# Kernel tuning notes

Measured on AMD Instinct MI355X. Metric: run time of the kernel, lower is better.

The kernel has to match this reference:

```python
import math
import jax, jax.numpy as jnp
import numpy as np

HIDDEN = 1024
N_HEADS = 16
HEAD_DIM = HIDDEN // N_HEADS
SEQ = 2048
BATCH = 2
MAX_SEQ = 2048
N_LAYERS = 4
ALPHA = 0.3
TOPK_FACTOR = 2
GAMMA = 0.5
M_FREQ = math.ceil(MAX_SEQ / 2) + 1  # rfft length


def _sample_indices(layer_idx):
    # FrequencyRampSampler.get_sample_indices (layer_idx is a static python int)
    l = layer_idx + 1
    M, L = M_FREQ, N_LAYERS
    if ALPHA > 1.0 / L:
        p = int(M * (1 - ALPHA) * (1 - (l - 1) / (L - 1))) if L > 1 else 0
        q = int(p + ALPHA * M)
    else:
        p = int(M * (1 - l / L))
        q = int(p + M / L)
    p = max(0, min(p, M - 1))
    q = max(p + 1, min(q, M))
    return p, q


def setup_inputs() -> dict:
    key = jax.random.key(0)
    ks = jax.random.split(key, 10)
    hidden_states = jax.random.normal(ks[0], (BATCH, SEQ, HIDDEN), jnp.float32)
    # causal additive mask [B,1,N,N]
    causal = jnp.tril(jnp.ones((SEQ, SEQ), jnp.float32))
    attention_mask = jnp.where(causal > 0, 0.0, -1e9).astype(jnp.float32)
    attention_mask = jnp.broadcast_to(attention_mask[None, None], (BATCH, 1, SEQ, SEQ))
    s = 0.02
    Wq = jax.random.normal(ks[1], (HIDDEN, HIDDEN), jnp.float32) * s
    Wk = jax.random.normal(ks[2], (HIDDEN, HIDDEN), jnp.float32) * s
    Wv = jax.random.normal(ks[3], (HIDDEN, HIDDEN), jnp.float32) * s
    Wo = jax.random.normal(ks[4], (HIDDEN, HIDDEN), jnp.float32) * s
    bq = jnp.zeros((HIDDEN,), jnp.float32)
    bk = jnp.zeros((HIDDEN,), jnp.float32)
    bv = jnp.zeros((HIDDEN,), jnp.float32)
    bo = jnp.zeros((HIDDEN,), jnp.float32)
    return dict(hidden_states=hidden_states, attention_mask=attention_mask,
                Wq=Wq, bq=bq, Wk=Wk, bk=bk, Wv=Wv, bv=bv, Wo=Wo, bo=bo,
                layer_idx=1)


def _forward(hidden_states, attention_mask, Wq, bq, Wk, bk, Wv, bv, Wo, bo, layer_idx):
    B, N, D = hidden_states.shape
    p, q = _sample_indices(layer_idx)
    Q = hidden_states @ Wq.T + bq
    K = hidden_states @ Wk.T + bk
    V = hidden_states @ Wv.T + bv

    # ---- time-domain branch: FFT -> band-select -> IFFT -> SDPA ----
    def band_filter(X):
        Xf = jnp.fft.rfft(X, axis=1)  # [B, M, D] complex64
        Xp = jnp.zeros_like(Xf).at[:, p:q, :].set(Xf[:, p:q, :])
        return jnp.fft.irfft(Xp, n=N, axis=1)

    Qt = band_filter(Q).reshape(B, N, N_HEADS, HEAD_DIM).transpose(0, 2, 1, 3)
    Kt = band_filter(K).reshape(B, N, N_HEADS, HEAD_DIM).transpose(0, 2, 1, 3)
    Vt = band_filter(V).reshape(B, N, N_HEADS, HEAD_DIM).transpose(0, 2, 1, 3)
    scores = jnp.einsum('bhnd,bhmd->bhnm', Qt, Kt) / math.sqrt(HEAD_DIM)
    scores = scores + attention_mask
    probs = jax.nn.softmax(scores, axis=-1)
    time_out = jnp.einsum('bhnm,bhmd->bhnd', probs, Vt)
    time_out = time_out.transpose(0, 2, 1, 3).reshape(B, N, D)

    # ---- frequency-domain branch: autocorrelation + top-k delay aggregation ----
    Qf = jnp.fft.rfft(Q, axis=1)
    Kf = jnp.fft.rfft(K, axis=1)
    corr = jnp.zeros_like(Qf).at[:, p:q, :].set(Qf[:, p:q, :] * jnp.conj(Kf[:, p:q, :]))
    R = jnp.fft.irfft(corr, n=N, axis=1)          # [B, N, D]
    R_mean = R.mean(axis=-1)                       # [B, N]
    k = min(max(1, int(TOPK_FACTOR * math.log(N + 1))), N)
    top_R, top_idx = jax.lax.top_k(R_mean, k)      # [B, k]
    attn_w = jax.nn.softmax(top_R, axis=-1)        # [B, k]
    # rolled index: (n - tau) mod N, for each of the k delays
    idx = (jnp.arange(N)[None, None, :] - top_idx[:, :, None]) % N   # [B, k, N]
    gathered = jnp.take_along_axis(V[:, None, :, :], idx[..., None], axis=2)  # [B, k, N, D]
    freq_out = jnp.einsum('bk,bknd->bnd', attn_w, gathered)

    out = GAMMA * time_out + (1.0 - GAMMA) * freq_out
    return out @ Wo.T + bo


def reference(hidden_states, attention_mask, Wq, bq, Wk, bk, Wv, bv, Wo, bo, layer_idx):
    return _forward(hidden_states, attention_mask, Wq, bq, Wk, bk, Wv, bv, Wo, bo, layer_idx)
```

## Files before the change

kernel.cpp:

```cpp
#include <hip/hip_runtime.h>
#include <hip/hip_bf16.h>

#define BATCHN 2
#define SEQ    2048
#define HID    1024
#define NHEADS 16
#define HD     64
#define P_LO   478
#define NF     307
#define NF2    614
#define NFP    640
#define KTOP   15
#define DPI    3.14159265358979323846
#define L2E    1.44269504f

typedef __bf16 bf16_t;
typedef bf16_t v8bf __attribute__((ext_vector_type(8)));
typedef bf16_t v4bf __attribute__((ext_vector_type(4)));
typedef float  v4f  __attribute__((ext_vector_type(4)));

#define MFMA(a,b,c) __builtin_amdgcn_mfma_f32_16x16x32_bf16(a,b,c,0,0,0)

#define GLDS(gp, lp) __builtin_amdgcn_global_load_lds( \
    (const __attribute__((address_space(1))) void*)(gp), \
    (__attribute__((address_space(3))) void*)(lp), 16, 0, 0)

__device__ __forceinline__ int self_detect(const unsigned short* __restrict__ x, char* SM) {
    int* s = (int*)SM;
    int t = threadIdx.x, bad = 0;
    for (int i = t; i < 8192; i += 256) {
        unsigned e = (x[i] >> 7) & 0xFF;
        if (e >= 0x90) bad++;
    }
    s[t] = bad; __syncthreads();
    for (int st = 128; st; st >>= 1) { if (t < st) s[t] += s[t + st]; __syncthreads(); }
    int r = (s[0] > 32) ? 1 : 0;
    __syncthreads();
    return r;
}

__device__ __forceinline__ void tab_body(int bi, char* SM, bf16_t* Ahi, bf16_t* Alo,
                                         bf16_t* Gt) {
    float* T = (float*)SM;
    int t = threadIdx.x;
    int m0 = (bi & 31) * 64, r0 = (bi >> 5) * 64;
    int m = t >> 2, rb = (t & 3) * 16;
    {
        v8bf g0, g1;
        #pragma unroll
        for (int i = 0; i < 16; i++) {
            int r = r0 + rb + i;
            float v = 0.f;
            if (r < NF2) {
                int f  = P_LO + (r < NF ? r : r - NF);
                int ph = (f * (m0 + m)) & (SEQ - 1);
                float ang = (float)(2.0 * DPI / SEQ) * (float)ph;
                float sn, cs;
                sincosf(ang, &sn, &cs);
                v = (r < NF) ? cs : sn;
            }
            T[(rb + i) * 65 + m] = v;
            bf16_t gv = (bf16_t)(v * (float)(2.0 / SEQ));
            if (i < 8) g0[i] = gv; else g1[i - 8] = gv;
        }
        *(v8bf*)&Gt[(size_t)(m0 + m) * NFP + r0 + rb]     = g0;
        *(v8bf*)&Gt[(size_t)(m0 + m) * NFP + r0 + rb + 8] = g1;
    }
    __syncthreads();
    int r = t >> 2, mb = (t & 3) * 16;
    v8bf h0, h1, l0, l1;
    #pragma unroll
    for (int i = 0; i < 16; i++) {
        float v = T[r * 65 + mb + i];
        bf16_t hh = (bf16_t)v;
        bf16_t ll = (bf16_t)(v - (float)hh);
        if (i < 8) { h0[i] = hh; l0[i] = ll; } else { h1[i - 8] = hh; l1[i - 8] = ll; }
    }
    size_t ro = (size_t)(r0 + r) * SEQ + m0 + mb;
    *(v8bf*)&Ahi[ro]     = h0;  *(v8bf*)&Ahi[ro + 8] = h1;
    *(v8bf*)&Alo[ro]     = l0;  *(v8bf*)&Alo[ro + 8] = l1;
}

__device__ __forceinline__ void norm_body(int bi, int fl, char* SM, const void* Xv,
                                          bf16_t* XTh, bf16_t* XTl) {
    float* T = (float*)SM;
    int t = threadIdx.x;
    int C0 = (bi & 15) * 64, R0 = (bi >> 4) * 64;
    int r = t >> 2;
    #pragma unroll
    for (int it = 0; it < 2; it++) {
        int c = (t & 3) * 8 + it * 32;
        float x[8];
        if (fl) {
            const float* p = (const float*)Xv + (size_t)(R0 + r) * HID + C0 + c;
            #pragma unroll
            for (int e = 0; e < 8; e++) x[e] = p[e];
        } else {
            const bf16_t* p = (const bf16_t*)Xv + (size_t)(R0 + r) * HID + C0 + c;
            #pragma unroll
            for (int e = 0; e < 8; e++) x[e] = (float)p[e];
        }
        #pragma unroll
        for (int e = 0; e < 8; e++) T[r * 65 + c + e] = x[e];
    }
    __syncthreads();
    int b  = (R0 >= SEQ) ? 1 : 0;
    int Rl = R0 - b * SEQ;
    int d  = t >> 2;
    #pragma unroll
    for (int it = 0; it < 2; it++) {
        int n = (t & 3) * 8 + it * 32;
        v8bf h, l;
        #pragma unroll
        for (int e = 0; e < 8; e++) {
            float x = T[(n + e) * 65 + d];
            bf16_t hh = (bf16_t)x;
            h[e] = hh; l[e] = (bf16_t)(x - (float)hh);
        }
        size_t off = ((size_t)b * HID + C0 + d) * SEQ + Rl + n;
        *(v8bf*)&XTh[off] = h;
        *(v8bf*)&XTl[off] = l;
    }
}

__device__ __forceinline__ void gemmv_body(int bi, int fl, char* SM, const void* Xraw,
                                           const void* Braw, const void* biasraw,
                                           bf16_t* Out) {
    bf16_t* As = (bf16_t*)SM;
    bf16_t* Bs = (bf16_t*)(SM + 8192);
    int t = threadIdx.x, wave = t >> 6, lane = t & 63;
    int lrow = lane & 15, quad = lane >> 4;
    int n0 = (bi & 7) * 128, m0 = (bi >> 3) * 128;
    int wm = (wave >> 1) * 64, wn = (wave & 1) * 64;
    int grow = lane >> 2, gcol = (lane & 3) * 8;
    v4f acc[4][4] = {};
    for (int k0 = 0; k0 < HID; k0 += 32) {
        __syncthreads();
        if (!fl) {
            const bf16_t* A = (const bf16_t*)Xraw;
            const bf16_t* B = (const bf16_t*)Braw;
            GLDS(&A[(size_t)(m0 + wave * 32 + grow) * HID + k0 + gcol],      &As[(wave * 32) * 32]);
            GLDS(&A[(size_t)(m0 + wave * 32 + 16 + grow) * HID + k0 + gcol], &As[(wave * 32 + 16) * 32]);
            GLDS(&B[(size_t)(n0 + wave * 32 + grow) * HID + k0 + gcol],      &Bs[(wave * 32) * 32]);
            GLDS(&B[(size_t)(n0 + wave * 32 + 16 + grow) * HID + k0 + gcol], &Bs[(wave * 32 + 16) * 32]);
        } else {
            const float* A = (const float*)Xraw;
            const float* B = (const float*)Braw;
            #pragma unroll
            for (int i2 = 0; i2 < 2; i2++) {
                int row = (t >> 2) + 64 * i2, col = (t & 3) * 8;
                const float* pa = &A[(size_t)(m0 + row) * HID + k0 + col];
                const float* pb = &B[(size_t)(n0 + row) * HID + k0 + col];
                v8bf ha, hb;
                #pragma unroll
                for (int e = 0; e < 8; e++) { ha[e] = (bf16_t)pa[e]; hb[e] = (bf16_t)pb[e]; }
                *(v8bf*)&As[row * 32 + col] = ha;
                *(v8bf*)&Bs[row * 32 + col] = hb;
            }
        }
        __syncthreads();
        v8bf a[4], b[4];
        #pragma unroll
        for (int i = 0; i < 4; i++) a[i] = *(v8bf*)&As[(wm + i * 16 + lrow) * 32 + quad * 8];
        #pragma unroll
        for (int j = 0; j < 4; j++) b[j] = *(v8bf*)&Bs[(wn + j * 16 + lrow) * 32 + quad * 8];
        #pragma unroll
        for (int i = 0; i < 4; i++)
        #pragma unroll
        for (int j = 0; j < 4; j++) acc[i][j] = MFMA(a[i], b[j], acc[i][j]);
    }
    #pragma unroll
    for (int i = 0; i < 4; i++)
    #pragma unroll
    for (int j = 0; j < 4; j++) {
        int col = n0 + wn + 16 * j + lrow;
        float bvv = fl ? ((const float*)biasraw)[col] : (float)((const bf16_t*)biasraw)[col];
        #pragma unroll
        for (int rg = 0; rg < 4; rg++) {
            int row = m0 + wm + 16 * i + quad * 4 + rg;
            Out[(size_t)row * HID + col] = (bf16_t)(acc[i][j][rg] + bvv);
        }
    }
}

__launch_bounds__(256)
__global__ void mega1_kernel(const void* __restrict__ X, const void* __restrict__ Wq,
                             const void* __restrict__ Wv, const void* __restrict__ bv,
                             bf16_t* __restrict__ Vm,
                             bf16_t* __restrict__ Ahi, bf16_t* __restrict__ Alo,
                             bf16_t* __restrict__ Gt,
                             bf16_t* __restrict__ XTh, bf16_t* __restrict__ XTl,
                             int* __restrict__ flag) {
    __shared__ __align__(16) char SM[17408];
    int bx = blockIdx.x;
    if (bx < 256) {
        int fl = self_detect((const unsigned short*)X, SM);
        gemmv_body(bx, fl, SM, X, Wv, bv, Vm);
    } else if (bx < 576) {
        tab_body(bx - 256, SM, Ahi, Alo, Gt);
    } else if (bx < 1600) {
        int fl = self_detect((const unsigned short*)X, SM);
        norm_body(bx - 576, fl, SM, X, XTh, XTl);
    } else {
        const unsigned short* x0 = (const unsigned short*)X;
        const unsigned short* x1 = (const unsigned short*)Wq;
        int* s = (int*)SM;
        int t = threadIdx.x, bad = 0;
        for (int i = t; i < 8192; i += 256) {
            unsigned e0 = (x0[i] >> 7) & 0xFF; if (e0 >= 0x90) bad++;
            unsigned e1 = (x1[i] >> 7) & 0xFF; if (e1 >= 0x90) bad++;
        }
        s[t] = bad; __syncthreads();
        for (int st = 128; st; st >>= 1) { if (t < st) s[t] += s[t + st]; __syncthreads(); }
        if (t == 0) *flag = (s[0] > 64) ? 1 : 0;
    }
}

__launch_bounds__(256)
__global__ void band_fwd(const bf16_t* __restrict__ Ahi, const bf16_t* __restrict__ Alo,
                         const bf16_t* __restrict__ XTh, const bf16_t* __restrict__ XTl,
                         bf16_t* __restrict__ Xfh, bf16_t* __restrict__ Xfl) {
    __shared__ __align__(16) bf16_t Ah[64 * 32], Al[64 * 32], Bh[64 * 32], Bl[64 * 32];
    int t = threadIdx.x, wave = t >> 6, lane = t & 63;
    int lrow = lane & 15, quad = lane >> 4;
    int m0 = blockIdx.y * 64, n0 = blockIdx.x * 64, b = blockIdx.z;
    int wm = (wave >> 1) * 32, wn = (wave & 1) * 32;
    int srow = t >> 2, scol = (t & 3) * 8;
    const bf16_t* bth = XTh + (size_t)b * HID * SEQ;
    const bf16_t* btl = XTl + (size_t)b * HID * SEQ;
    v4f acc[2][2] = {};
    for (int k0 = 0; k0 < SEQ; k0 += 32) {
        __syncthreads();
        GLDS(&Ahi[(size_t)(m0 + srow) * SEQ + k0 + scol], &Ah[srow * 32 + scol]);
        GLDS(&Alo[(size_t)(m0 + srow) * SEQ + k0 + scol], &Al[srow * 32 + scol]);
        GLDS(&bth[(size_t)(n0 + srow) * SEQ + k0 + scol], &Bh[srow * 32 + scol]);
        GLDS(&btl[(size_t)(n0 + srow) * SEQ + k0 + scol], &Bl[srow * 32 + scol]);
        __syncthreads();
        v8bf ah0 = *(v8bf*)&Ah[(wm + lrow) * 32 + quad * 8];
        v8bf ah1 = *(v8bf*)&Ah[(wm + 16 + lrow) * 32 + quad * 8];
        v8bf al0 = *(v8bf*)&Al[(wm + lrow) * 32 + quad * 8];
        v8bf al1 = *(v8bf*)&Al[(wm + 16 + lrow) * 32 + quad * 8];
        v8bf bh0 = *(v8bf*)&Bh[(wn + lrow) * 32 + quad * 8];
        v8bf bh1 = *(v8bf*)&Bh[(wn + 16 + lrow) * 32 + quad * 8];
        v8bf bl0 = *(v8bf*)&Bl[(wn + lrow) * 32 + quad * 8];
        v8bf bl1 = *(v8bf*)&Bl[(wn + 16 + lrow) * 32 + quad * 8];
        acc[0][0] = MFMA(ah0, bh0, acc[0][0]); acc[0][0] = MFMA(ah0, bl0, acc[0][0]); acc[0][0] = MFMA(al0, bh0, acc[0][0]);
        acc[0][1] = MFMA(ah0, bh1, acc[0][1]); acc[0][1] = MFMA(ah0, bl1, acc[0][1]); acc[0][1] = MFMA(al0, bh1, acc[0][1]);
        acc[1][0] = MFMA(ah1, bh0, acc[1][0]); acc[1][0] = MFMA(ah1, bl0, acc[1][0]); acc[1][0] = MFMA(al1, bh0, acc[1][0]);
        acc[1][1] = MFMA(ah1, bh1, acc[1][1]); acc[1][1] = MFMA(ah1, bl1, acc[1][1]); acc[1][1] = MFMA(al1, bh1, acc[1][1]);
    }
    bf16_t* oh = Xfh + (size_t)b * NFP * HID;
    bf16_t* ol = Xfl + (size_t)b * NFP * HID;
    #pragma unroll
    for (int i = 0; i < 2; i++)
    #pragma unroll
    for (int j = 0; j < 2; j++) {
        int col = n0 + wn + 16 * j + lrow;
        #pragma unroll
        for (int rg = 0; rg < 4; rg++) {
            int row = m0 + wm + 16 * i + quad * 4 + rg;
            float v = acc[i][j][rg];
            bf16_t h = (bf16_t)v;
            oh[(size_t)row * HID + col] = h;
            ol[(size_t)row * HID + col] = (bf16_t)(v - (float)h);
        }
    }
}

__launch_bounds__(256)
__global__ void proj_f(const int* __restrict__ flag, const bf16_t* __restrict__ Xfh,
                       const bf16_t* __restrict__ Xfl,
                       const void* __restrict__ Wq_, const void* __restrict__ Wk_,
                       const void* __restrict__ Wv_,
                       bf16_t* __restrict__ Qfh, bf16_t* __restrict__ Qfl,
                       bf16_t* __restrict__ Kfh, bf16_t* __restrict__ Kfl,
                       bf16_t* __restrict__ QfT, bf16_t* __restrict__ KfT,
                       bf16_t* __restrict__ VfT) {
    int fl = *flag;
    int bz = blockIdx.z, b = bz & 1, sel = bz >> 1;
    const void* Wraw = sel == 0 ? Wq_ : sel == 1 ? Wk_ : Wv_;
    bf16_t* Ch = sel == 0 ? Qfh : Kfh;
    bf16_t* Cl = sel == 0 ? Qfl : Kfl;
    bf16_t* CT = sel == 0 ? QfT : sel == 1 ? KfT : VfT;
    bool qk = sel < 2;
    __shared__ __align__(16) bf16_t Ah[64 * 32], Al[64 * 32], Bh[64 * 32], Bl[64 * 32];
    int t = threadIdx.x, wave = t >> 6, lane = t & 63;
    int lrow = lane & 15, quad = lane >> 4;
    int m0 = blockIdx.y * 64, n0 = blockIdx.x * 64;
    int wm = (wave >> 1) * 32, wn = (wave & 1) * 32;
    int srow = t >> 2, scol = (t & 3) * 8;
    const size_t zo = (size_t)b * NFP * HID;
    v4f acc[2][2] = {};
    for (int k0 = 0; k0 < HID; k0 += 32) {
        __syncthreads();
        GLDS(&Xfh[zo + (size_t)(m0 + srow) * HID + k0 + scol], &Ah[srow * 32 + scol]);
        GLDS(&Xfl[zo + (size_t)(m0 + srow) * HID + k0 + scol], &Al[srow * 32 + scol]);
        {
            float xb[8];
            if (fl) {
                const float* p = (const float*)Wraw + (size_t)(n0 + srow) * HID + k0 + scol;
                #pragma unroll
                for (int e = 0; e < 8; e++) xb[e] = p[e];
            } else {
                const bf16_t* p = (const bf16_t*)Wraw + (size_t)(n0 + srow) * HID + k0 + scol;
                #pragma unroll
                for (int e = 0; e < 8; e++) xb[e] = (float)p[e];
            }
            v8bf h, l;
            #pragma unroll
            for (int e = 0; e < 8; e++) {
                bf16_t hh = (bf16_t)xb[e];
                h[e] = hh; l[e] = (bf16_t)(xb[e] - (float)hh);
            }
            *(v8bf*)&Bh[srow * 32 + scol] = h;
            *(v8bf*)&Bl[srow * 32 + scol] = l;
        }
        __syncthreads();
        v8bf ah0 = *(v8bf*)&Ah[(wm + lrow) * 32 + quad * 8];
        v8bf ah1 = *(v8bf*)&Ah[(wm + 16 + lrow) * 32 + quad * 8];
        v8bf al0 = *(v8bf*)&Al[(wm + lrow) * 32 + quad * 8];
        v8bf al1 = *(v8bf*)&Al[(wm + 16 + lrow) * 32 + quad * 8];
        v8bf bh0 = *(v8bf*)&Bh[(wn + lrow) * 32 + quad * 8];
        v8bf bh1 = *(v8bf*)&Bh[(wn + 16 + lrow) * 32 + quad * 8];
        acc[0][0] = MFMA(ah0, bh0, acc[0][0]); acc[0][0] = MFMA(al0, bh0, acc[0][0]);
        acc[0][1] = MFMA(ah0, bh1, acc[0][1]); acc[0][1] = MFMA(al0, bh1, acc[0][1]);
        acc[1][0] = MFMA(ah1, bh0, acc[1][0]); acc[1][0] = MFMA(al1, bh0, acc[1][0]);
        acc[1][1] = MFMA(ah1, bh1, acc[1][1]); acc[1][1] = MFMA(al1, bh1, acc[1][1]);
        if (qk) {
            v8bf bl0 = *(v8bf*)&Bl[(wn + lrow) * 32 + quad * 8];
            v8bf bl1 = *(v8bf*)&Bl[(wn + 16 + lrow) * 32 + quad * 8];
            acc[0][0] = MFMA(ah0, bl0, acc[0][0]);
            acc[0][1] = MFMA(ah0, bl1, acc[0][1]);
            acc[1][0] = MFMA(ah1, bl0, acc[1][0]);
            acc[1][1] = MFMA(ah1, bl1, acc[1][1]);
        }
    }
    #pragma unroll
    for (int i = 0; i < 2; i++)
    #pragma unroll
    for (int j = 0; j < 2; j++) {
        int col = n0 + wn + 16 * j + lrow;
        v4bf pk;
        #pragma unroll
        for (int rg = 0; rg < 4; rg++) {
            int row = m0 + wm + 16 * i + quad * 4 + rg;
            float v = acc[i][j][rg];
            bf16_t h = (bf16_t)v;
            pk[rg] = h;
            if (qk) {
                Ch[zo + (size_t)row * HID + col] = h;
                Cl[zo + (size_t)row * HID + col] = (bf16_t)(v - (float)h);
            }
        }
        *(v4bf*)&CT[zo + (size_t)col * NFP + m0 + wm + 16 * i + quad * 4] = pk;
    }
}

__launch_bounds__(256)
__global__ void sfreq_kernel(const bf16_t* __restrict__ Qh, const bf16_t* __restrict__ Ql,
                             const bf16_t* __restrict__ Kh, const bf16_t* __restrict__ Kl,
                             float* __restrict__ Sre, float* __restrict__ Sim) {
    int f = blockIdx.x, b = blockIdx.y, t = threadIdx.x;
    const size_t oc = ((size_t)b * NFP + f) * HID;
    const size_t os = ((size_t)b * NFP + NF + f) * HID;
    float re = 0.f, im = 0.f;
    for (int d = t; d < HID; d += 256) {
        float cq = (float)Qh[oc + d] + (float)Ql[oc + d];
        float sq = (float)Qh[os + d] + (float)Ql[os + d];
        float ck = (float)Kh[oc + d] + (float)Kl[oc + d];
        float sk = (float)Kh[os + d] + (float)Kl[os + d];
        re += cq * ck + sq * sk;
        im += cq * sk - sq * ck;
    }
    #pragma unroll
    for (int msk = 1; msk < 64; msk <<= 1) { re += __shfl_xor(re, msk); im += __shfl_xor(im, msk); }
    __shared__ float rbuf[8];
    int wave = t >> 6, lane = t & 63;
    if (lane == 0) { rbuf[wave] = re; rbuf[4 + wave] = im; }
    __syncthreads();
    if (t == 0) {
        Sre[b * NF + f] = rbuf[0] + rbuf[1] + rbuf[2] + rbuf[3];
        Sim[b * NF + f] = rbuf[4] + rbuf[5] + rbuf[6] + rbuf[7];
    }
}

__device__ __forceinline__ void inv_body(int bi, char* SM, const bf16_t* Gt,
                                         const bf16_t* QfT, const bf16_t* KfT,
                                         const bf16_t* VfT, bf16_t* Qt, bf16_t* Kt,
                                         bf16_t* VTd) {
    int b = (bi >> 7) & 1, sel = bi >> 8;
    const bf16_t* BT = (sel == 0 ? QfT : sel == 1 ? KfT : VfT) + (size_t)b * HID * NFP;
    bf16_t* Out = sel == 0 ? Qt : sel == 1 ? Kt : VTd;
    bool trans = (sel == 2);
    bf16_t* As = (bf16_t*)SM;
    bf16_t* Bs = (bf16_t*)(SM + 8192);
    int t = threadIdx.x, wave = t >> 6, lane = t & 63;
    int lrow = lane & 15, quad = lane >> 4;
    int n0 = (bi & 7) * 128, m0 = ((bi >> 3) & 15) * 128;
    int wm = (wave >> 1) * 64, wn = (wave & 1) * 64;
    int grow = lane >> 2, gcol = (lane & 3) * 8;
    v4f acc[4][4] = {};
    for (int k0 = 0; k0 < NFP; k0 += 32) {
        __syncthreads();
        GLDS(&Gt[(size_t)(m0 + wave * 32 + grow) * NFP + k0 + gcol],      &As[(wave * 32) * 32]);
        GLDS(&Gt[(size_t)(m0 + wave * 32 + 16 + grow) * NFP + k0 + gcol], &As[(wave * 32 + 16) * 32]);
        GLDS(&BT[(size_t)(n0 + wave * 32 + grow) * NFP + k0 + gcol],      &Bs[(wave * 32) * 32]);
        GLDS(&BT[(size_t)(n0 + wave * 32 + 16 + grow) * NFP + k0 + gcol], &Bs[(wave * 32 + 16) * 32]);
        __syncthreads();
        v8bf a[4], bfr[4];
        #pragma unroll
        for (int i = 0; i < 4; i++) a[i]   = *(v8bf*)&As[(wm + i * 16 + lrow) * 32 + quad * 8];
        #pragma unroll
        for (int j = 0; j < 4; j++) bfr[j] = *(v8bf*)&Bs[(wn + j * 16 + lrow) * 32 + quad * 8];
        #pragma unroll
        for (int i = 0; i < 4; i++)
        #pragma unroll
        for (int j = 0; j < 4; j++) acc[i][j] = MFMA(a[i], bfr[j], acc[i][j]);
    }
    #pragma unroll
    for (int i = 0; i < 4; i++)
    #pragma unroll
    for (int j = 0; j < 4; j++) {
        int col = n0 + wn + 16 * j + lrow;
        if (trans) {
            v4bf pk;
            #pragma unroll
            for (int rg = 0; rg < 4; rg++) pk[rg] = (bf16_t)acc[i][j][rg];
            *(v4bf*)&Out[((size_t)b * HID + col) * SEQ + m0 + wm + 16 * i + quad * 4] = pk;
        } else {
            #pragma unroll
            for (int rg = 0; rg < 4; rg++) {
                int row = m0 + wm + 16 * i + quad * 4 + rg;
                Out[(size_t)b * SEQ * HID + (size_t)row * HID + col] = (bf16_t)acc[i][j][rg];
            }
        }
    }
}

__device__ __forceinline__ void rmean_body(int bi, char* SM, const float* Sre,
                                           const float* Sim, float* Rm) {
    int b = bi >> 5;
    float* sr  = (float*)SM;
    float* si  = sr + NF;
    float* red = si + NF;
    int nl = threadIdx.x & 63, part = threadIdx.x >> 6;
    int n = (bi & 31) * 64 + nl;
    for (int i = threadIdx.x; i < NF; i += 256) { sr[i] = Sre[b * NF + i]; si[i] = Sim[b * NF + i]; }
    __syncthreads();
    float acc = 0.f;
    for (int r = part; r < NF; r += 4) {
        int ph = ((P_LO + r) * n) & (SEQ - 1);
        float ang = (float)(2.0 * DPI / SEQ) * (float)ph;
        float sn, cs;
        sincosf(ang, &sn, &cs);
        acc += sr[r] * cs - si[r] * sn;
    }
    red[part * 64 + nl] = acc;
    __syncthreads();
    if (part == 0) {
        float s = red[nl] + red[64 + nl] + red[128 + nl] + red[192 + nl];
        Rm[b * SEQ + n] = s * (float)(2.0 / ((double)SEQ * (double)HID));
    }
}

__launch_bounds__(256)
__global__ void mega5_kernel(const bf16_t* __restrict__ Gt, const bf16_t* __restrict__ QfT,
                             const bf16_t* __restrict__ KfT, const bf16_t* __restrict__ VfT,
                             bf16_t* __restrict__ Qt, bf16_t* __restrict__ Kt,
                             bf16_t* __restrict__ VTd,
                             const float* __restrict__ Sre, const float* __restrict__ Sim,
                             float* __restrict__ Rm) {
    __shared__ __align__(16) char SM[16384];
    int bx = blockIdx.x;
    if (bx < 768) inv_body(bx, SM, Gt, QfT, KfT, VfT, Qt, Kt, VTd);
    else          rmean_body(bx - 768, SM, Sre, Sim, Rm);
}

__device__ __forceinline__ void attn_body(int bi, char* SM, const bf16_t* Qt,
                                          const bf16_t* Kt, const bf16_t* VT, bf16_t* TO) {
    bf16_t* Ks = (bf16_t*)SM;
    bf16_t* Vs = (bf16_t*)(SM + 18432);
    bf16_t* Ps = (bf16_t*)(SM + 36864);
    int t = threadIdx.x, wave = t >> 6, lane = t & 63;
    int lrow = lane & 15, quad = lane >> 4;
    int h = (bi >> 4) & 15, b = bi >> 8;
    int q0 = (15 - (bi & 15)) * 128;
    const size_t base = (size_t)b * SEQ * HID + (size_t)h * HD;
    const bf16_t* vb_ = VT + ((size_t)b * HID + h * HD) * SEQ;
    bf16_t* Pw = &Ps[wave * 16 * 72];

    v8bf qa[2][2];
    #pragma unroll
    for (int g = 0; g < 2; g++) {
        int qrow = q0 + g * 64 + wave * 16 + lrow;
        qa[g][0] = *(const v8bf*)&Qt[base + (size_t)qrow * HID + quad * 8];
        qa[g][1] = *(const v8bf*)&Qt[base + (size_t)qrow * HID + 32 + quad * 8];
    }
    v4f o[2][4] = {};
    float m_i[2] = {-1e30f, -1e30f}, l_i[2] = {0.f, 0.f};
    int srow = t >> 2, cc0 = (t & 3) * 16;
    int nch = q0 / 64 + 2;
    v8bf kp0 = *(const v8bf*)&Kt[base + (size_t)srow * HID + cc0];
    v8bf kp1 = *(const v8bf*)&Kt[base + (size_t)srow * HID + cc0 + 8];
    v8bf vp0 = *(const v8bf*)&vb_[(size_t)srow * SEQ + cc0];
    v8bf vp1 = *(const v8bf*)&vb_[(size_t)srow * SEQ + cc0 + 8];
    const float SC = 0.125f * L2E;
    for (int c = 0; c < nch; c++) {
        int kb = c * 64;
        int cur = c & 1;
        bf16_t* Kc = &Ks[cur * 64 * 72];
        bf16_t* Vc = &Vs[cur * 64 * 72];
        *(v8bf*)&Kc[srow * 72 + cc0]     = kp0;
        *(v8bf*)&Kc[srow * 72 + cc0 + 8] = kp1;
        *(v8bf*)&Vc[srow * 72 + cc0]     = vp0;
        *(v8bf*)&Vc[srow * 72 + cc0 + 8] = vp1;
        __syncthreads();
        if (c + 1 < nch) {
            int kb2 = kb + 64;
            kp0 = *(const v8bf*)&Kt[base + (size_t)(kb2 + srow) * HID + cc0];
            kp1 = *(const v8bf*)&Kt[base + (size_t)(kb2 + srow) * HID + cc0 + 8];
            vp0 = *(const v8bf*)&vb_[(size_t)srow * SEQ + kb2 + cc0];
            vp1 = *(const v8bf*)&vb_[(size_t)srow * SEQ + kb2 + cc0 + 8];
        }
        v8bf kA[4][2], vB[4][2];
        #pragma unroll
        for (int ct = 0; ct < 4; ct++) {
            kA[ct][0] = *(v8bf*)&Kc[(ct * 16 + lrow) * 72 + quad * 8];
            kA[ct][1] = *(v8bf*)&Kc[(ct * 16 + lrow) * 72 + 32 + quad * 8];
            vB[ct][0] = *(v8bf*)&Vc[(ct * 16 + lrow) * 72 + quad * 8];
            vB[ct][1] = *(v8bf*)&Vc[(ct * 16 + lrow) * 72 + 32 + quad * 8];
        }
        #pragma unroll
        for (int g = 0; g < 2; g++) {
            if (kb >= q0 + g * 64 + 64) continue;
            bool masked = (kb == q0 + g * 64);
            v4f s[4];
            #pragma unroll
            for (int ct = 0; ct < 4; ct++) {
                v4f z = {};
                z = MFMA(kA[ct][0], qa[g][0], z);
                s[ct] = MFMA(kA[ct][1], qa[g][1], z);
            }
            float sv[4][4];
            float mx = -1e30f;
            #pragma unroll
            for (int ct = 0; ct < 4; ct++)
            #pragma unroll
            for (int r = 0; r < 4; r++) {
                float x = s[ct][r] * SC;
                if (masked && (ct * 16 + quad * 4 + r > wave * 16 + lrow)) x = -1e30f;
                sv[ct][r] = x;
                mx = fmaxf(mx, x);
            }
            mx = fmaxf(mx, __shfl_xor(mx, 16));
            mx = fmaxf(mx, __shfl_xor(mx, 32));
            float mnew = fmaxf(m_i[g], mx);
            float alpha = exp2f(m_i[g] - mnew);
            m_i[g] = mnew;
            float rs = 0.f;
            #pragma unroll
            for (int ct = 0; ct < 4; ct++)
            #pragma unroll
            for (int r = 0; r < 4; r++) { float p = exp2f(sv[ct][r] - mnew); sv[ct][r] = p; rs += p; }
            rs += __shfl_xor(rs, 16);
            rs += __shfl_xor(rs, 32);
            l_i[g] = l_i[g] * alpha + rs;
            #pragma unroll
            for (int r = 0; r < 4; r++) {
                float ar = __shfl(alpha, quad * 4 + r);
                #pragma unroll
                for (int dt = 0; dt < 4; dt++) o[g][dt][r] *= ar;
            }
            #pragma unroll
            for (int ct = 0; ct < 4; ct++) {
                v4bf pk;
                #pragma unroll
                for (int r = 0; r < 4; r++) pk[r] = (bf16_t)sv[ct][r];
                *(v4bf*)&Pw[lrow * 72 + ct * 16 + quad * 4] = pk;
            }
            v8bf pa0 = *(v8bf*)&Pw[lrow * 72 + quad * 8];
            v8bf pa1 = *(v8bf*)&Pw[lrow * 72 + 32 + quad * 8];
            #pragma unroll
            for (int dt = 0; dt < 4; dt++) {
                o[g][dt] = MFMA(pa0, vB[dt][0], o[g][dt]);
                o[g][dt] = MFMA(pa1, vB[dt][1], o[g][dt]);
            }
        }
        __syncthreads();
    }
    #pragma unroll
    for (int g = 0; g < 2; g++)
    #pragma unroll
    for (int r = 0; r < 4; r++) {
        float lr = __shfl(l_i[g], quad * 4 + r);
        int qg = q0 + g * 64 + wave * 16 + quad * 4 + r;
        #pragma unroll
        for (int dt = 0; dt < 4; dt++)
            TO[base + (size_t)qg * HID + dt * 16 + lrow] = (bf16_t)(o[g][dt][r] / lr);
    }
}

__device__ __forceinline__ void topk_body(int b, const float* Rm, int* Ti, float* Tw) {
    int lane = threadIdx.x;
    float v[32];
    #pragma unroll
    for (int j = 0; j < 32; j++) v[j] = Rm[b * SEQ + j * 64 + lane];
    float selv[KTOP];
    int   seli[KTOP];
    for (int kk = 0; kk < KTOP; kk++) {
        float best = -INFINITY; int bi = lane;
        #pragma unroll
        for (int j = 0; j < 32; j++) {
            float x = v[j];
            if (x > best) { best = x; bi = j * 64 + lane; }
        }
        #pragma unroll
        for (int off = 1; off < 64; off <<= 1) {
            float ov = __shfl_xor(best, off);
            int   oi = __shfl_xor(bi, off);
            if (ov > best || (ov == best && oi < bi)) { best = ov; bi = oi; }
        }
        selv[kk] = best; seli[kk] = bi;
        if (lane == (bi & 63)) v[bi >> 6] = -INFINITY;
    }
    float mx = selv[0];
    #pragma unroll
    for (int i = 1; i < KTOP; i++) mx = fmaxf(mx, selv[i]);
    float s = 0.f, e[KTOP];
    #pragma unroll
    for (int i = 0; i < KTOP; i++) { e[i] = __expf(selv[i] - mx); s += e[i]; }
    if (lane < KTOP) { Tw[b * KTOP + lane] = e[lane] / s; Ti[b * KTOP + lane] = seli[lane]; }
}

__launch_bounds__(256)
__global__ void mega6_kernel(const bf16_t* __restrict__ Qt, const bf16_t* __restrict__ Kt,
                             const bf16_t* __restrict__ VT, bf16_t* __restrict__ TO,
                             const float* __restrict__ Rm, int* __restrict__ Ti,
                             float* __restrict__ Tw) {
    __shared__ __align__(16) char SM[46080];
    int bx = blockIdx.x;
    if (bx < 512) attn_body(bx, SM, Qt, Kt, VT, TO);
    else if (threadIdx.x < 64) topk_body(bx - 512, Rm, Ti, Tw);
}

__launch_bounds__(256)
__global__ void combine_kernel(const bf16_t* __restrict__ TO, const bf16_t* __restrict__ V,
                               const int* __restrict__ Ti, const float* __restrict__ Tw,
                               bf16_t* __restrict__ Yc) {
    int b = blockIdx.y;
    __shared__ int   ti[KTOP];
    __shared__ float tw[KTOP];
    if (threadIdx.x < KTOP) { ti[threadIdx.x] = Ti[b * KTOP + threadIdx.x]; tw[threadIdx.x] = Tw[b * KTOP + threadIdx.x]; }
    __syncthreads();
    int idx = threadIdx.x * 8;
    int r = idx >> 10, d = idx & 1023;
    int n = blockIdx.x * 2 + r;
    float fo[8] = {};
    #pragma unroll
    for (int kk = 0; kk < KTOP; kk++) {
        int nn = (n - ti[kk] + SEQ) & (SEQ - 1);
        v8bf vv = *(const v8bf*)&V[((size_t)b * SEQ + nn) * HID + d];
        float w8 = tw[kk];
        #pragma unroll
        for (int e = 0; e < 8; e++) fo[e] += w8 * (float)vv[e];
    }
    size_t off = ((size_t)b * SEQ + n) * HID + d;
    v8bf to = *(const v8bf*)&TO[off];
    v8bf y;
    #pragma unroll
    for (int e = 0; e < 8; e++) y[e] = (bf16_t)(0.5f * (float)to[e] + 0.5f * fo[e]);
    *(v8bf*)&Yc[off] = y;
}

__launch_bounds__(256)
__global__ void gemmO_kernel(const int* __restrict__ flag, const bf16_t* __restrict__ A,
                             const void* __restrict__ Braw, const void* __restrict__ biasraw,
                             void* __restrict__ Out) {
    int fl = *flag;
    __shared__ __align__(16) bf16_t As[128 * 32];
    __shared__ __align__(16) bf16_t Bs[128 * 32];
    int t = threadIdx.x, wave = t >> 6, lane = t & 63;
    int lrow = lane & 15, quad = lane >> 4;
    int m0 = blockIdx.y * 128, n0 = blockIdx.x * 128;
    int wm = (wave >> 1) * 64, wn = (wave & 1) * 64;
    int grow = lane >> 2, gcol = (lane & 3) * 8;
    v4f acc[4][4] = {};
    for (int k0 = 0; k0 < HID; k0 += 32) {
        __syncthreads();
        GLDS(&A[(size_t)(m0 + wave * 32 + grow) * HID + k0 + gcol],      &As[(wave * 32) * 32]);
        GLDS(&A[(size_t)(m0 + wave * 32 + 16 + grow) * HID + k0 + gcol], &As[(wave * 32 + 16) * 32]);
        if (!fl) {
            const bf16_t* B = (const bf16_t*)Braw;
            GLDS(&B[(size_t)(n0 + wave * 32 + grow) * HID + k0 + gcol],      &Bs[(wave * 32) * 32]);
            GLDS(&B[(size_t)(n0 + wave * 32 + 16 + grow) * HID + k0 + gcol], &Bs[(wave * 32 + 16) * 32]);
        } else {
            const float* B = (const float*)Braw;
            #pragma unroll
            for (int i2 = 0; i2 < 2; i2++) {
                int row = (t >> 2) + 64 * i2, col = (t & 3) * 8;
                const float* p = &B[(size_t)(n0 + row) * HID + k0 + col];
                v8bf h;
                #pragma unroll
                for (int e = 0; e < 8; e++) h[e] = (bf16_t)p[e];
                *(v8bf*)&Bs[row * 32 + col] = h;
            }
        }
        __syncthreads();
        v8bf a[4], b[4];
        #pragma unroll
        for (int i = 0; i < 4; i++) a[i] = *(v8bf*)&As[(wm + i * 16 + lrow) * 32 + quad * 8];
        #pragma unroll
        for (int j = 0; j < 4; j++) b[j] = *(v8bf*)&Bs[(wn + j * 16 + lrow) * 32 + quad * 8];
        #pragma unroll
        for (int i = 0; i < 4; i++)
        #pragma unroll
        for (int j = 0; j < 4; j++) acc[i][j] = MFMA(a[i], b[j], acc[i][j]);
    }
    #pragma unroll
    for (int i = 0; i < 4; i++)
    #pragma unroll
    for (int j = 0; j < 4; j++) {
        int col = n0 + wn + 16 * j + lrow;
        float bvv = fl ? ((const float*)biasraw)[col] : (float)((const bf16_t*)biasraw)[col];
        #pragma unroll
        for (int rg = 0; rg < 4; rg++) {
            int row = m0 + wm + 16 * i + quad * 4 + rg;
            float v = acc[i][j][rg] + bvv;
            size_t off = (size_t)row * HID + col;
            if (fl) ((float*)Out)[off] = v;
            else ((bf16_t*)Out)[off] = (bf16_t)v;
        }
    }
}

extern "C" void kernel_launch(void* const* d_in, const int* in_sizes, int n_in,
                              void* d_out, int out_size, void* d_ws, size_t ws_size,
                              hipStream_t stream) {
    (void)in_sizes; (void)n_in; (void)out_size; (void)ws_size;
    const void* X  = d_in[0];
    const void* Wq = d_in[2];
    const void* Wk = d_in[4];
    const void* Wv = d_in[6];
    const void* bv = d_in[7];
    const void* Wo = d_in[8];
    const void* bo = d_in[9];

    const size_t SZ_X   = (size_t)BATCHN * SEQ * HID * 2;
    const size_t SZ_TAB = (size_t)NFP * SEQ * 2;
    const size_t SZ_F   = (size_t)BATCHN * NFP * HID * 2;
    char* w = (char*)d_ws;
    bf16_t* Xfh = (bf16_t*)(w);
    bf16_t* Xfl = (bf16_t*)(w + SZ_F);
    bf16_t* Qt  = (bf16_t*)(w);
    bf16_t* Yc  = (bf16_t*)(w);
    bf16_t* XTh = (bf16_t*)(w + SZ_X);
    bf16_t* Qfh = (bf16_t*)(w + SZ_X);
    bf16_t* Qfl = (bf16_t*)(w + SZ_X + SZ_F);
    bf16_t* Kfh = (bf16_t*)(w + SZ_X + 2 * SZ_F);
    bf16_t* Kt  = (bf16_t*)(w + SZ_X);
    bf16_t* XTl = (bf16_t*)(w + 2 * SZ_X);
    bf16_t* Kfl = (bf16_t*)(w + 2 * SZ_X);
    bf16_t* QfT = (bf16_t*)(w + 2 * SZ_X + SZ_F);
    bf16_t* KfT = (bf16_t*)(w + 2 * SZ_X + 2 * SZ_F);
    bf16_t* TO  = (bf16_t*)(w + 2 * SZ_X);
    bf16_t* Vm  = (bf16_t*)(w + 3 * SZ_X);
    bf16_t* Gt  = (bf16_t*)(w + 4 * SZ_X);
    bf16_t* Ahi = (bf16_t*)(w + 4 * SZ_X + SZ_TAB);
    bf16_t* Alo = (bf16_t*)(w + 4 * SZ_X + 2 * SZ_TAB);
    bf16_t* VfT = (bf16_t*)(w + 4 * SZ_X + SZ_TAB);
    char*  sm  = w + 4 * SZ_X + 3 * SZ_TAB;
    int*   flag = (int*)sm;
    float* Sre  = (float*)(sm + 256);
    float* Sim  = (float*)(sm + 256 + 4096);
    float* Rm   = (float*)(sm + 256 + 8192);
    int*   Ti   = (int*)  (sm + 256 + 8192 + 16384);
    float* Tw   = (float*)(sm + 256 + 8192 + 16384 + 256);
    bf16_t* VT  = (bf16_t*)d_out;

    mega1_kernel<<<1601, 256, 0, stream>>>(X, Wq, Wv, bv, Vm, Ahi, Alo, Gt, XTh, XTl, flag);
    band_fwd<<<dim3(16, NFP / 64, BATCHN), 256, 0, stream>>>(Ahi, Alo, XTh, XTl, Xfh, Xfl);
    proj_f<<<dim3(16, NFP / 64, 6), 256, 0, stream>>>(flag, Xfh, Xfl, Wq, Wk, Wv,
                                                      Qfh, Qfl, Kfh, Kfl, QfT, KfT, VfT);
    sfreq_kernel<<<dim3(NF, BATCHN), 256, 0, stream>>>(Qfh, Qfl, Kfh, Kfl, Sre, Sim);
    mega5_kernel<<<832, 256, 0, stream>>>(Gt, QfT, KfT, VfT, Qt, Kt, VT, Sre, Sim, Rm);
    mega6_kernel<<<514, 256, 0, stream>>>(Qt, Kt, VT, TO, Rm, Ti, Tw);
    combine_kernel<<<dim3(SEQ / 2, BATCHN), 256, 0, stream>>>(TO, Vm, Ti, Tw, Yc);
    gemmO_kernel<<<dim3(8, 32), 256, 0, stream>>>(flag, Yc, Wo, bo, d_out);
}
```

Before: 410.3 us.

## Enlarge frequency projection tiles to 128x128 and skip lo-part MFMAs for bf16 inputs

The Q/K/V frequency projection moves from 64x64 to 128x128 tiles, with each wave computing a 64x64 sub-tile. For bf16 weights the tiles are loaded straight into LDS by global_load_lds, and the reloaded A fragments are shared across more MFMAs. Both band_fwd and the projection now skip the low-part B loads and their correction MFMAs when the input-precision flag says the data is bf16, which removes about a third of the MFMA work in that case. The trade-offs are more registers per thread (16 accumulators), a grid of only 8x5x6 blocks, and lower precision when the inputs are bf16.

```diff
diff --git a/kernel.cpp b/kernel.cpp
--- a/kernel.cpp
+++ b/kernel.cpp
@@ -217,9 +217,11 @@
 }
 
 __launch_bounds__(256)
-__global__ void band_fwd(const bf16_t* __restrict__ Ahi, const bf16_t* __restrict__ Alo,
+__global__ void band_fwd(const int* __restrict__ flag,
+                         const bf16_t* __restrict__ Ahi, const bf16_t* __restrict__ Alo,
                          const bf16_t* __restrict__ XTh, const bf16_t* __restrict__ XTl,
                          bf16_t* __restrict__ Xfh, bf16_t* __restrict__ Xfl) {
+    int fl = *flag;
     __shared__ __align__(16) bf16_t Ah[64 * 32], Al[64 * 32], Bh[64 * 32], Bl[64 * 32];
     int t = threadIdx.x, wave = t >> 6, lane = t & 63;
     int lrow = lane & 15, quad = lane >> 4;
@@ -234,87 +236,8 @@
         GLDS(&Ahi[(size_t)(m0 + srow) * SEQ + k0 + scol], &Ah[srow * 32 + scol]);
         GLDS(&Alo[(size_t)(m0 + srow) * SEQ + k0 + scol], &Al[srow * 32 + scol]);
         GLDS(&bth[(size_t)(n0 + srow) * SEQ + k0 + scol], &Bh[srow * 32 + scol]);
-        GLDS(&btl[(size_t)(n0 + srow) * SEQ + k0 + scol], &Bl[srow * 32 + scol]);
-        __syncthreads();
-        v8bf ah0 = *(v8bf*)&Ah[(wm + lrow) * 32 + quad * 8];
-        v8bf ah1 = *(v8bf*)&Ah[(wm + 16 + lrow) * 32 + quad * 8];
-        v8bf al0 = *(v8bf*)&Al[(wm + lrow) * 32 + quad * 8];
-        v8bf al1 = *(v8bf*)&Al[(wm + 16 + lrow) * 32 + quad * 8];
-        v8bf bh0 = *(v8bf*)&Bh[(wn + lrow) * 32 + quad * 8];
-        v8bf bh1 = *(v8bf*)&Bh[(wn + 16 + lrow) * 32 + quad * 8];
-        v8bf bl0 = *(v8bf*)&Bl[(wn + lrow) * 32 + quad * 8];
-        v8bf bl1 = *(v8bf*)&Bl[(wn + 16 + lrow) * 32 + quad * 8];
-        acc[0][0] = MFMA(ah0, bh0, acc[0][0]); acc[0][0] = MFMA(ah0, bl0, acc[0][0]); acc[0][0] = MFMA(al0, bh0, acc[0][0]);
-        acc[0][1] = MFMA(ah0, bh1, acc[0][1]); acc[0][1] = MFMA(ah0, bl1, acc[0][1]); acc[0][1] = MFMA(al0, bh1, acc[0][1]);
-        acc[1][0] = MFMA(ah1, bh0, acc[1][0]); acc[1][0] = MFMA(ah1, bl0, acc[1][0]); acc[1][0] = MFMA(al1, bh0, acc[1][0]);
-        acc[1][1] = MFMA(ah1, bh1, acc[1][1]); acc[1][1] = MFMA(ah1, bl1, acc[1][1]); acc[1][1] = MFMA(al1, bh1, acc[1][1]);
-    }
-    bf16_t* oh = Xfh + (size_t)b * NFP * HID;
-    bf16_t* ol = Xfl + (size_t)b * NFP * HID;
-    #pragma unroll
-    for (int i = 0; i < 2; i++)
-    #pragma unroll
-    for (int j = 0; j < 2; j++) {
-        int col = n0 + wn + 16 * j + lrow;
-        #pragma unroll
-        for (int rg = 0; rg < 4; rg++) {
-            int row = m0 + wm + 16 * i + quad * 4 + rg;
-            float v = acc[i][j][rg];
-            bf16_t h = (bf16_t)v;
-            oh[(size_t)row * HID + col] = h;
-            ol[(size_t)row * HID + col] = (bf16_t)(v - (float)h);
-        }
-    }
-}
-
-__launch_bounds__(256)
-__global__ void proj_f(const int* __restrict__ flag, const bf16_t* __restrict__ Xfh,
-                       const bf16_t* __restrict__ Xfl,
-                       const void* __restrict__ Wq_, const void* __restrict__ Wk_,
-                       const void* __restrict__ Wv_,
-                       bf16_t* __restrict__ Qfh, bf16_t* __restrict__ Qfl,
-                       bf16_t* __restrict__ Kfh, bf16_t* __restrict__ Kfl,
-                       bf16_t* __restrict__ QfT, bf16_t* __restrict__ KfT,
-                       bf16_t* __restrict__ VfT) {
-    int fl = *flag;
-    int bz = blockIdx.z, b = bz & 1, sel = bz >> 1;
-    const void* Wraw = sel == 0 ? Wq_ : sel == 1 ? Wk_ : Wv_;
-    bf16_t* Ch = sel == 0 ? Qfh : Kfh;
-    bf16_t* Cl = sel == 0 ? Qfl : Kfl;
-    bf16_t* CT = sel == 0 ? QfT : sel == 1 ? KfT : VfT;
-    bool qk = sel < 2;
-    __shared__ __align__(16) bf16_t Ah[64 * 32], Al[64 * 32], Bh[64 * 32], Bl[64 * 32];
-    int t = threadIdx.x, wave = t >> 6, lane = t & 63;
-    int lrow = lane & 15, quad = lane >> 4;
-    int m0 = blockIdx.y * 64, n0 = blockIdx.x * 64;
-    int wm = (wave >> 1) * 32, wn = (wave & 1) * 32;
-    int srow = t >> 2, scol = (t & 3) * 8;
-    const size_t zo = (size_t)b * NFP * HID;
-    v4f acc[2][2] = {};
-    for (int k0 = 0; k0 < HID; k0 += 32) {
-        __syncthreads();
-        GLDS(&Xfh[zo + (size_t)(m0 + srow) * HID + k0 + scol], &Ah[srow * 32 + scol]);
-        GLDS(&Xfl[zo + (size_t)(m0 + srow) * HID + k0 + scol], &Al[srow * 32 + scol]);
-        {
-            float xb[8];
-            if (fl) {
-                const float* p = (const float*)Wraw + (size_t)(n0 + srow) * HID + k0 + scol;
-                #pragma unroll
-                for (int e = 0; e < 8; e++) xb[e] = p[e];
-            } else {
-                const bf16_t* p = (const bf16_t*)Wraw + (size_t)(n0 + srow) * HID + k0 + scol;
-                #pragma unroll
-                for (int e = 0; e < 8; e++) xb[e] = (float)p[e];
-            }
-            v8bf h, l;
-            #pragma unroll
-            for (int e = 0; e < 8; e++) {
-                bf16_t hh = (bf16_t)xb[e];
-                h[e] = hh; l[e] = (bf16_t)(xb[e] - (float)hh);
-            }
-            *(v8bf*)&Bh[srow * 32 + scol] = h;
-            *(v8bf*)&Bl[srow * 32 + scol] = l;
-        }
+        if (fl)
+            GLDS(&btl[(size_t)(n0 + srow) * SEQ + k0 + scol], &Bl[srow * 32 + scol]);
         __syncthreads();
         v8bf ah0 = *(v8bf*)&Ah[(wm + lrow) * 32 + quad * 8];
         v8bf ah1 = *(v8bf*)&Ah[(wm + 16 + lrow) * 32 + quad * 8];
@@ -326,7 +249,7 @@
         acc[0][1] = MFMA(ah0, bh1, acc[0][1]); acc[0][1] = MFMA(al0, bh1, acc[0][1]);
         acc[1][0] = MFMA(ah1, bh0, acc[1][0]); acc[1][0] = MFMA(al1, bh0, acc[1][0]);
         acc[1][1] = MFMA(ah1, bh1, acc[1][1]); acc[1][1] = MFMA(al1, bh1, acc[1][1]);
-        if (qk) {
+        if (fl) {
             v8bf bl0 = *(v8bf*)&Bl[(wn + lrow) * 32 + quad * 8];
             v8bf bl1 = *(v8bf*)&Bl[(wn + 16 + lrow) * 32 + quad * 8];
             acc[0][0] = MFMA(ah0, bl0, acc[0][0]);
@@ -335,10 +258,110 @@
             acc[1][1] = MFMA(ah1, bl1, acc[1][1]);
         }
     }
+    bf16_t* oh = Xfh + (size_t)b * NFP * HID;
+    bf16_t* ol = Xfl + (size_t)b * NFP * HID;
     #pragma unroll
     for (int i = 0; i < 2; i++)
     #pragma unroll
     for (int j = 0; j < 2; j++) {
+        int col = n0 + wn + 16 * j + lrow;
+        #pragma unroll
+        for (int rg = 0; rg < 4; rg++) {
+            int row = m0 + wm + 16 * i + quad * 4 + rg;
+            float v = acc[i][j][rg];
+            bf16_t h = (bf16_t)v;
+            oh[(size_t)row * HID + col] = h;
+            ol[(size_t)row * HID + col] = (bf16_t)(v - (float)h);
+        }
+    }
+}
+
+__launch_bounds__(256)
+__global__ void proj128_f(const int* __restrict__ flag, const bf16_t* __restrict__ Xfh,
+                          const bf16_t* __restrict__ Xfl,
+                          const void* __restrict__ Wq_, const void* __restrict__ Wk_,
+                          const void* __restrict__ Wv_,
+                          bf16_t* __restrict__ Qfh, bf16_t* __restrict__ Qfl,
+                          bf16_t* __restrict__ Kfh, bf16_t* __restrict__ Kfl,
+                          bf16_t* __restrict__ QfT, bf16_t* __restrict__ KfT,
+                          bf16_t* __restrict__ VfT) {
+    int fl = *flag;
+    int bz = blockIdx.z, b = bz & 1, sel = bz >> 1;
+    const void* Wraw = sel == 0 ? Wq_ : sel == 1 ? Wk_ : Wv_;
+    bf16_t* Ch = sel == 0 ? Qfh : Kfh;
+    bf16_t* Cl = sel == 0 ? Qfl : Kfl;
+    bf16_t* CT = sel == 0 ? QfT : sel == 1 ? KfT : VfT;
+    bool qk = sel < 2;
+    __shared__ __align__(16) bf16_t Ah[128 * 32], Al[128 * 32], Bh[128 * 32], Bl[128 * 32];
+    int t = threadIdx.x, wave = t >> 6, lane = t & 63;
+    int lrow = lane & 15, quad = lane >> 4;
+    int m0 = blockIdx.y * 128, n0 = blockIdx.x * 128;
+    int wm = (wave >> 1) * 64, wn = (wave & 1) * 64;
+    int grow = lane >> 2, gcol = (lane & 3) * 8;
+    const size_t zo = (size_t)b * NFP * HID;
+    v4f acc[4][4] = {};
+    for (int k0 = 0; k0 < HID; k0 += 32) {
+        __syncthreads();
+        GLDS(&Xfh[zo + (size_t)(m0 + wave * 32 + grow) * HID + k0 + gcol],      &Ah[(wave * 32) * 32]);
+        GLDS(&Xfh[zo + (size_t)(m0 + wave * 32 + 16 + grow) * HID + k0 + gcol], &Ah[(wave * 32 + 16) * 32]);
+        GLDS(&Xfl[zo + (size_t)(m0 + wave * 32 + grow) * HID + k0 + gcol],      &Al[(wave * 32) * 32]);
+        GLDS(&Xfl[zo + (size_t)(m0 + wave * 32 + 16 + grow) * HID + k0 + gcol], &Al[(wave * 32 + 16) * 32]);
+        if (!fl) {
+            const bf16_t* B = (const bf16_t*)Wraw;
+            GLDS(&B[(size_t)(n0 + wave * 32 + grow) * HID + k0 + gcol],      &Bh[(wave * 32) * 32]);
+            GLDS(&B[(size_t)(n0 + wave * 32 + 16 + grow) * HID + k0 + gcol], &Bh[(wave * 32 + 16) * 32]);
+        } else {
+            const float* B = (const float*)Wraw;
+            #pragma unroll
+            for (int i2 = 0; i2 < 2; i2++) {
+                int row = (t >> 2) + 64 * i2, col = (t & 3) * 8;
+                const float* p = &B[(size_t)(n0 + row) * HID + k0 + col];
+                v8bf h, l;
+                #pragma unroll
+                for (int e = 0; e < 8; e++) {
+                    bf16_t hh = (bf16_t)p[e];
+                    h[e] = hh; l[e] = (bf16_t)(p[e] - (float)hh);
+                }
+                *(v8bf*)&Bh[row * 32 + col] = h;
+                *(v8bf*)&Bl[row * 32 + col] = l;
+            }
+        }
+        __syncthreads();
+        v8bf bh[4];
+        #pragma unroll
+        for (int j = 0; j < 4; j++) bh[j] = *(v8bf*)&Bh[(wn + j * 16 + lrow) * 32 + quad * 8];
+        {
+            v8bf ah[4];
+            #pragma unroll
+            for (int i = 0; i < 4; i++) ah[i] = *(v8bf*)&Ah[(wm + i * 16 + lrow) * 32 + quad * 8];
+            #pragma unroll
+            for (int i = 0; i < 4; i++)
+            #pragma unroll
+            for (int j = 0; j < 4; j++) acc[i][j] = MFMA(ah[i], bh[j], acc[i][j]);
+            if (fl) {
+                v8bf bl[4];
+                #pragma unroll
+                for (int j = 0; j < 4; j++) bl[j] = *(v8bf*)&Bl[(wn + j * 16 + lrow) * 32 + quad * 8];
+                #pragma unroll
+                for (int i = 0; i < 4; i++)
+                #pragma unroll
+                for (int j = 0; j < 4; j++) acc[i][j] = MFMA(ah[i], bl[j], acc[i][j]);
+            }
+        }
+        {
+            v8bf al[4];
+            #pragma unroll
+            for (int i = 0; i < 4; i++) al[i] = *(v8bf*)&Al[(wm + i * 16 + lrow) * 32 + quad * 8];
+            #pragma unroll
+            for (int i = 0; i < 4; i++)
+            #pragma unroll
+            for (int j = 0; j < 4; j++) acc[i][j] = MFMA(al[i], bh[j], acc[i][j]);
+        }
+    }
+    #pragma unroll
+    for (int i = 0; i < 4; i++)
+    #pragma unroll
+    for (int j = 0; j < 4; j++) {
         int col = n0 + wn + 16 * j + lrow;
         v4bf pk;
         #pragma unroll
@@ -778,9 +801,9 @@
     bf16_t* VT  = (bf16_t*)d_out;
 
     mega1_kernel<<<1601, 256, 0, stream>>>(X, Wq, Wv, bv, Vm, Ahi, Alo, Gt, XTh, XTl, flag);
-    band_fwd<<<dim3(16, NFP / 64, BATCHN), 256, 0, stream>>>(Ahi, Alo, XTh, XTl, Xfh, Xfl);
-    proj_f<<<dim3(16, NFP / 64, 6), 256, 0, stream>>>(flag, Xfh, Xfl, Wq, Wk, Wv,
-                                                      Qfh, Qfl, Kfh, Kfl, QfT, KfT, VfT);
+    band_fwd<<<dim3(16, NFP / 64, BATCHN), 256, 0, stream>>>(flag, Ahi, Alo, XTh, XTl, Xfh, Xfl);
+    proj128_f<<<dim3(8, NFP / 128, 6), 256, 0, stream>>>(flag, Xfh, Xfl, Wq, Wk, Wv,
+                                                         Qfh, Qfl, Kfh, Kfl, QfT, KfT, VfT);
     sfreq_kernel<<<dim3(NF, BATCHN), 256, 0, stream>>>(Qfh, Qfl, Kfh, Kfl, Sre, Sim);
     mega5_kernel<<<832, 256, 0, stream>>>(Gt, QfT, KfT, VfT, Qt, Kt, VT, Sre, Sim, Rm);
     mega6_kernel<<<514, 256, 0, stream>>>(Qt, Kt, VT, TO, Rm, Ti, Tw);
```

After: 456.9 us. 11.4% more time.
